# Optimization experiments

Hardware: AMD Instinct MI355X
Metric: run time of the kernel (lower is better)

## Reference

```python
import jax, jax.numpy as jnp
import numpy as np

NUM_HEADS = 8
NUM_LEVELS = 4
NUM_POINTS = 4
EMBED = 256
HEAD_DIM = EMBED // NUM_HEADS
SPATIAL = [(100, 100), (50, 50), (25, 25), (13, 13)]  # (H, W) per level


def _bilinear_sample(val, grid):
    """torch.nn.functional.grid_sample(mode='bilinear', padding_mode='zeros', align_corners=False).
    val: [B, H, W, C], grid: [B, N, 2] with (x, y) in [-1, 1]. Returns [B, N, C]."""
    B, H, W, C = val.shape
    x = (grid[..., 0] + 1.0) * (W * 0.5) - 0.5
    y = (grid[..., 1] + 1.0) * (H * 0.5) - 0.5
    x0 = jnp.floor(x)
    y0 = jnp.floor(y)
    wx1 = x - x0
    wy1 = y - y0
    wx0 = 1.0 - wx1
    wy0 = 1.0 - wy1
    x0i = x0.astype(jnp.int32)
    y0i = y0.astype(jnp.int32)
    valf = val.reshape(B, H * W, C)

    def corner(xi, yi, w):
        valid = (xi >= 0) & (xi < W) & (yi >= 0) & (yi < H)
        idx = jnp.clip(yi, 0, H - 1) * W + jnp.clip(xi, 0, W - 1)
        v = jnp.take_along_axis(valf, idx[..., None], axis=1)  # [B, N, C]
        return v * (w * valid)[..., None]

    return (corner(x0i, y0i, wx0 * wy0) + corner(x0i + 1, y0i, wx1 * wy0)
            + corner(x0i, y0i + 1, wx0 * wy1) + corner(x0i + 1, y0i + 1, wx1 * wy1))


def setup_inputs() -> dict:
    key = jax.random.key(0)
    ks = jax.random.split(key, 12)
    bs, nq = 4, 6000
    nv = sum(h * w for h, w in SPATIAL)
    s = 0.02
    return {
        "query": jax.random.normal(ks[0], (bs, nq, EMBED), jnp.float32),
        "value": jax.random.normal(ks[1], (bs, nv, EMBED), jnp.float32),
        "reference_points": jax.random.uniform(ks[2], (bs, nq, NUM_LEVELS, 2), jnp.float32),
        "W_off": jax.random.normal(ks[3], (EMBED, NUM_HEADS * NUM_LEVELS * NUM_POINTS * 2), jnp.float32) * s,
        "b_off": jax.random.normal(ks[4], (NUM_HEADS * NUM_LEVELS * NUM_POINTS * 2,), jnp.float32),
        "W_attn": jax.random.normal(ks[5], (EMBED, NUM_HEADS * NUM_LEVELS * NUM_POINTS), jnp.float32) * s,
        "b_attn": jnp.zeros((NUM_HEADS * NUM_LEVELS * NUM_POINTS,), jnp.float32),
        "W_val": jax.random.normal(ks[6], (EMBED, EMBED), jnp.float32) * s,
        "b_val": jnp.zeros((EMBED,), jnp.float32),
        "W_out": jax.random.normal(ks[7], (EMBED, EMBED), jnp.float32) * s,
        "b_out": jnp.zeros((EMBED,), jnp.float32),
        "spatial_shapes": jnp.asarray(np.array(SPATIAL, dtype=np.int32)),
    }


def reference(query, value, reference_points, W_off, b_off, W_attn, b_attn,
              W_val, b_val, W_out, b_out, spatial_shapes):
    shapes = [(int(h), int(w)) for h, w in np.asarray(spatial_shapes)]
    bs, nq, _ = query.shape
    nv = value.shape[1]

    v = (value @ W_val + b_val).reshape(bs, nv, NUM_HEADS, HEAD_DIM)
    offsets = (query @ W_off + b_off).reshape(bs, nq, NUM_HEADS, NUM_LEVELS, NUM_POINTS, 2)
    aw = (query @ W_attn + b_attn).reshape(bs, nq, NUM_HEADS, NUM_LEVELS * NUM_POINTS)
    aw = jax.nn.softmax(aw, axis=-1).reshape(bs, nq, NUM_HEADS, NUM_LEVELS, NUM_POINTS)

    # offset normalizer is [W, H] per level
    norm = jnp.asarray([[w, h] for h, w in shapes], dtype=query.dtype)  # [L, 2]
    loc = reference_points[:, :, None, :, None, :] + offsets / norm[None, None, None, :, None, :]
    grids = 2.0 * loc - 1.0  # [bs, nq, H, L, P, 2]
    # -> [bs*H, nq*P, 2] per level
    grids = jnp.transpose(grids, (0, 2, 1, 3, 4, 5)).reshape(bs * NUM_HEADS, nq, NUM_LEVELS, NUM_POINTS, 2)

    v_bh = jnp.transpose(v, (0, 2, 1, 3)).reshape(bs * NUM_HEADS, nv, HEAD_DIM)
    sampled = []
    start = 0
    for l, (H_, W_) in enumerate(shapes):
        val_l = v_bh[:, start:start + H_ * W_].reshape(bs * NUM_HEADS, H_, W_, HEAD_DIM)
        grid_l = grids[:, :, l].reshape(bs * NUM_HEADS, nq * NUM_POINTS, 2)
        s_l = _bilinear_sample(val_l, grid_l).reshape(bs * NUM_HEADS, nq, NUM_POINTS, HEAD_DIM)
        sampled.append(s_l)
        start += H_ * W_
    sampled = jnp.stack(sampled, axis=2)  # [bs*H, nq, L, P, c]

    aw_bh = jnp.transpose(aw, (0, 2, 1, 3, 4)).reshape(bs * NUM_HEADS, nq, NUM_LEVELS, NUM_POINTS)
    out = (sampled * aw_bh[..., None]).sum(axis=(2, 3))  # [bs*H, nq, c]
    out = out.reshape(bs, NUM_HEADS, nq, HEAD_DIM).transpose(0, 2, 1, 3).reshape(bs, nq, EMBED)
    out = out @ W_out + b_out
    return out + query
```

## Files before the change

kernel.cpp:

```cpp
#include <hip/hip_runtime.h>
#include <hip/hip_bf16.h>

#define BS 4
#define NQ 6000
#define NV 13294
#define NH 8
#define HD 32
#define EMB 256
#define MV (BS * NV)
#define MQ (BS * NQ)

typedef __attribute__((ext_vector_type(8))) short short8;
typedef __attribute__((ext_vector_type(4))) float floatx4;

__device__ __constant__ float LVL_DIM[4] = {100.f, 50.f, 25.f, 13.f};

__device__ inline unsigned short bf16bits(float f) {
  __hip_bfloat16 h = __float2bfloat16(f);
  return *reinterpret_cast<unsigned short*>(&h);
}
__device__ inline unsigned int pk2bf(float lo, float hi) {
  return (unsigned int)bf16bits(lo) | ((unsigned int)bf16bits(hi) << 16);
}
__device__ inline float bflo(unsigned int u) { return __uint_as_float(u << 16); }
__device__ inline float bfhi(unsigned int u) { return __uint_as_float(u & 0xffff0000u); }

#define LDSTR 40
#define TILEU (128 * LDSTR)

__global__ __launch_bounds__(256) void wtrans_kernel(
    const float* __restrict__ W_val, const float* __restrict__ W_off,
    const float* __restrict__ W_attn, const float* __restrict__ W_out,
    unsigned short* __restrict__ Wt_val, unsigned short* __restrict__ Wt_qcat,
    unsigned short* __restrict__ Wt_out) {
  __shared__ float tile[32][33];
  const int b = blockIdx.x;
  const int x = threadIdx.x & 31, ty = threadIdx.x >> 5;

  const float* src;
  unsigned short* dst;
  int k0, n0;
  if (b < 64) {
    src = W_val;
    dst = Wt_val;
    k0 = (b >> 3) * 32;
    n0 = (b & 7) * 32;
  } else if (b < 128) {
    const int bb = b - 64;
    src = W_off;
    dst = Wt_qcat;
    k0 = (bb >> 3) * 32;
    n0 = (bb & 7) * 32;
  } else if (b < 160) {
    const int bb = b - 128;
    src = W_attn;
    dst = Wt_qcat + 256 * EMB;
    k0 = (bb >> 2) * 32;
    n0 = (bb & 3) * 32;
#pragma unroll
    for (int i = 0; i < 4; ++i)
      tile[ty + 8 * i][x] = src[(size_t)(k0 + ty + 8 * i) * 128 + n0 + x];
    __syncthreads();
#pragma unroll
    for (int i = 0; i < 4; ++i)
      dst[(size_t)(n0 + ty + 8 * i) * EMB + k0 + x] =
          bf16bits(tile[x][ty + 8 * i]);
    return;
  } else {
    const int bb = b - 160;
    src = W_out;
    dst = Wt_out;
    k0 = (bb >> 3) * 32;
    n0 = (bb & 7) * 32;
  }
#pragma unroll
  for (int i = 0; i < 4; ++i)
    tile[ty + 8 * i][x] = src[(size_t)(k0 + ty + 8 * i) * 256 + n0 + x];
  __syncthreads();
#pragma unroll
  for (int i = 0; i < 4; ++i)
    dst[(size_t)(n0 + ty + 8 * i) * EMB + k0 + x] = bf16bits(tile[x][ty + 8 * i]);
}

__device__ inline void loadA32(const float* __restrict__ A, int M, int m0,
                               int k0, int tid, float4 ra[4]) {
  const int r = tid >> 1, kh = (tid & 1) * 16;
  const int row = m0 + r;
  if (row < M) {
    const float* src = A + (size_t)row * EMB + k0 + kh;
#pragma unroll
    for (int j = 0; j < 4; ++j) ra[j] = *(const float4*)(src + 4 * j);
  } else {
#pragma unroll
    for (int j = 0; j < 4; ++j) ra[j] = make_float4(0.f, 0.f, 0.f, 0.f);
  }
}
__device__ inline void storeA32(unsigned short* lds, int tid,
                                const float4 ra[4]) {
  const int r = tid >> 1, kh = (tid & 1) * 16;
  unsigned short* dst = lds + r * LDSTR + kh;
  uint4 u0, u1;
  u0.x = pk2bf(ra[0].x, ra[0].y);
  u0.y = pk2bf(ra[0].z, ra[0].w);
  u0.z = pk2bf(ra[1].x, ra[1].y);
  u0.w = pk2bf(ra[1].z, ra[1].w);
  u1.x = pk2bf(ra[2].x, ra[2].y);
  u1.y = pk2bf(ra[2].z, ra[2].w);
  u1.z = pk2bf(ra[3].x, ra[3].y);
  u1.w = pk2bf(ra[3].z, ra[3].w);
  *(uint4*)(dst) = u0;
  *(uint4*)(dst + 8) = u1;
}
__device__ inline void loadBb(const unsigned short* __restrict__ B, int NB,
                              int n0, int k0, int tid, uint4 rb[2]) {
  const int r = tid >> 1, kh = (tid & 1) * 16;
  const int row = n0 + r;
  if (row < NB) {
    const unsigned short* src = B + (size_t)row * EMB + k0 + kh;
    rb[0] = *(const uint4*)(src);
    rb[1] = *(const uint4*)(src + 8);
  } else {
    rb[0] = make_uint4(0, 0, 0, 0);
    rb[1] = make_uint4(0, 0, 0, 0);
  }
}
__device__ inline void storeBb(unsigned short* lds, int tid,
                               const uint4 rb[2]) {
  const int r = tid >> 1, kh = (tid & 1) * 16;
  unsigned short* dst = lds + r * LDSTR + kh;
  *(uint4*)(dst) = rb[0];
  *(uint4*)(dst + 8) = rb[1];
}

__device__ inline void mfma_step32(const unsigned short* ldsA,
                                   const unsigned short* ldsB, int wm, int wn,
                                   int lane, floatx4 acc[4][4]) {
  const unsigned short* ap =
      ldsA + (wm * 64 + (lane & 15)) * LDSTR + (lane >> 4) * 8;
  const unsigned short* bp =
      ldsB + (wn * 64 + (lane & 15)) * LDSTR + (lane >> 4) * 8;
  short8 af[4], bfr[4];
#pragma unroll
  for (int t = 0; t < 4; ++t) {
    af[t] = *(const short8*)(ap + t * 16 * LDSTR);
    bfr[t] = *(const short8*)(bp + t * 16 * LDSTR);
  }
#pragma unroll
  for (int mt = 0; mt < 4; ++mt)
#pragma unroll
    for (int nt = 0; nt < 4; ++nt)
      acc[mt][nt] = __builtin_amdgcn_mfma_f32_16x16x32_bf16(af[mt], bfr[nt],
                                                            acc[mt][nt], 0, 0, 0);
}

__device__ inline void gemm_loop32_f32A(const float* __restrict__ A, int M,
                                        int m0,
                                        const unsigned short* __restrict__ B,
                                        int NB, int n0, unsigned short* lds,
                                        int tid, int wm, int wn, int lane,
                                        floatx4 acc[4][4]) {
  unsigned short* bufA[2] = {lds, lds + 2 * TILEU};
  unsigned short* bufB[2] = {lds + TILEU, lds + 3 * TILEU};
  float4 sa[2][4];
  uint4 sb[2][2];
  loadA32(A, M, m0, 0, tid, sa[0]);
  loadBb(B, NB, n0, 0, tid, sb[0]);
  loadA32(A, M, m0, 32, tid, sa[1]);
  loadBb(B, NB, n0, 32, tid, sb[1]);
  storeA32(bufA[0], tid, sa[0]);
  storeBb(bufB[0], tid, sb[0]);
  __syncthreads();
#pragma unroll
  for (int k = 0; k < 8; ++k) {
    const int cur = k & 1, nxt = cur ^ 1;
    if (k + 2 < 8) {
      loadA32(A, M, m0, (k + 2) * 32, tid, sa[k & 1]);
      loadBb(B, NB, n0, (k + 2) * 32, tid, sb[k & 1]);
    }
    if (k + 1 < 8) {
      storeA32(bufA[nxt], tid, sa[(k + 1) & 1]);
      storeBb(bufB[nxt], tid, sb[(k + 1) & 1]);
    }
    mfma_step32(bufA[cur], bufB[cur], wm, wn, lane, acc);
    __syncthreads();
  }
}

__device__ inline void gemm_loop32_bf16A(const unsigned short* __restrict__ A,
                                         int M, int m0,
                                         const unsigned short* __restrict__ B,
                                         int NB, int n0, unsigned short* lds,
                                         int tid, int wm, int wn, int lane,
                                         floatx4 acc[4][4]) {
  unsigned short* bufA[2] = {lds, lds + 2 * TILEU};
  unsigned short* bufB[2] = {lds + TILEU, lds + 3 * TILEU};
  uint4 sa[2][2], sb[2][2];
  loadBb(A, M, m0, 0, tid, sa[0]);
  loadBb(B, NB, n0, 0, tid, sb[0]);
  loadBb(A, M, m0, 32, tid, sa[1]);
  loadBb(B, NB, n0, 32, tid, sb[1]);
  storeBb(bufA[0], tid, sa[0]);
  storeBb(bufB[0], tid, sb[0]);
  __syncthreads();
#pragma unroll
  for (int k = 0; k < 8; ++k) {
    const int cur = k & 1, nxt = cur ^ 1;
    if (k + 2 < 8) {
      loadBb(A, M, m0, (k + 2) * 32, tid, sa[k & 1]);
      loadBb(B, NB, n0, (k + 2) * 32, tid, sb[k & 1]);
    }
    if (k + 1 < 8) {
      storeBb(bufA[nxt], tid, sa[(k + 1) & 1]);
      storeBb(bufB[nxt], tid, sb[(k + 1) & 1]);
    }
    mfma_step32(bufA[cur], bufB[cur], wm, wn, lane, acc);
    __syncthreads();
  }
}

__global__ __launch_bounds__(256, 2) void vqproj_kernel(
    const float* __restrict__ value, const unsigned short* __restrict__ Wt_val,
    const float* __restrict__ b_val, unsigned short* __restrict__ vbh,
    const float* __restrict__ query, const unsigned short* __restrict__ Wt_qcat,
    const float* __restrict__ refpts, const float* __restrict__ b_off,
    const float* __restrict__ b_attn, float* __restrict__ locbuf,
    float* __restrict__ awbuf) {
  __shared__ unsigned short lds[4 * TILEU];
  const int tid = threadIdx.x, lane = tid & 63, w = tid >> 6;
  const int wm = w >> 1, wn = w & 1;
  floatx4 acc[4][4];
  const floatx4 zero = {0.f, 0.f, 0.f, 0.f};
#pragma unroll
  for (int i2 = 0; i2 < 4; i2++)
#pragma unroll
    for (int j = 0; j < 4; j++) acc[i2][j] = zero;
  const int quad = lane >> 4, cl = lane & 15;

  if (blockIdx.x < 832) {
    const int chunk = blockIdx.x >> 4, i = blockIdx.x & 15;
    const int m0 = (chunk * 8 + (i & 7)) * 128;
    const int n0 = (i >> 3) * 128;
    gemm_loop32_f32A(value, MV, m0, Wt_val, 256, n0, lds, tid, wm, wn, lane,
                     acc);
#pragma unroll
    for (int mt = 0; mt < 4; ++mt) {
#pragma unroll
      for (int r = 0; r < 4; ++r) {
        const int row = m0 + wm * 64 + mt * 16 + quad * 4 + r;
        if (row < MV) {
          const int b = row / NV, n = row - b * NV;
#pragma unroll
          for (int nt = 0; nt < 4; ++nt) {
            const int c = n0 + wn * 64 + nt * 16 + cl;
            const int h = c >> 5, d = c & 31;
            vbh[(((size_t)(b * NH + h)) * NV + n) * HD + d] =
                bf16bits(acc[mt][nt][r] + b_val[c]);
          }
        }
      }
    }
  } else {
    const int bid = blockIdx.x - 832;
    const int chunk = bid / 24, i = bid % 24;
    const int m_idx = chunk * 8 + (i & 7);
    if (m_idx >= 188) return;
    const int m0 = m_idx * 128;
    const int n0 = (i >> 3) * 128;
    gemm_loop32_f32A(query, MQ, m0, Wt_qcat, 384, n0, lds, tid, wm, wn, lane,
                     acc);
    if (n0 < 256) {
#pragma unroll
      for (int mt = 0; mt < 4; ++mt) {
#pragma unroll
        for (int r = 0; r < 4; ++r) {
          const int row = m0 + wm * 64 + mt * 16 + quad * 4 + r;
          if (row < MQ) {
#pragma unroll
            for (int nt = 0; nt < 4; ++nt) {
              const int c = n0 + wn * 64 + nt * 16 + cl;
              const int xy = c & 1, l = (c >> 3) & 3;
              const float dim = LVL_DIM[l];
              const float ref = refpts[(size_t)row * 8 + l * 2 + xy];
              locbuf[(size_t)row * 256 + c] =
                  ref * dim + acc[mt][nt][r] + b_off[c] - 0.5f;
            }
          }
        }
      }
    } else {
#pragma unroll
      for (int mt = 0; mt < 4; ++mt) {
#pragma unroll
        for (int r = 0; r < 4; ++r) {
          const int row = m0 + wm * 64 + mt * 16 + quad * 4 + r;
          if (row < MQ) {
#pragma unroll
            for (int nt = 0; nt < 4; ++nt) {
              const int ca = wn * 64 + nt * 16 + cl;
              awbuf[(size_t)row * 128 + ca] = acc[mt][nt][r] + b_attn[ca];
            }
          }
        }
      }
    }
  }
}

__global__ __launch_bounds__(256, 4) void sample_kernel(
    const unsigned short* __restrict__ vbh, const float* __restrict__ locbuf,
    const float* __restrict__ awbuf, unsigned short* __restrict__ sampledb) {
  const int blk = blockIdx.x;
  const int t = blk >> 3;
  const int quarter = t / 375;
  const int j = t - quarter * 375;
  const int slice = (blk & 7) * 4 + quarter;
  const int h = slice & 7;
  const int w = threadIdx.x >> 6;
  const int lane = threadIdx.x & 63;
  const int r0 = (slice >> 3) * NQ + j * 16 + w * 4;
  const int g = lane >> 2;
  const int d8 = lane & 3;
  const int l = g >> 2;

  const int W_ = (l < 2) ? ((l == 0) ? 100 : 50) : ((l == 2) ? 25 : 13);
  const int START = (l < 2) ? ((l == 0) ? 0 : 10000) : ((l == 2) ? 12500 : 13125);
  const unsigned int* base =
      (const unsigned int*)vbh + ((size_t)slice * NV + START) * 16 + d8 * 4;

  float acc[4][8];
#pragma unroll
  for (int rr = 0; rr < 4; ++rr) {
    const int row = r0 + rr;
    const float2 xy =
        *(const float2*)(locbuf + (size_t)row * 256 + h * 32 + g * 2);
    const float wl = awbuf[(size_t)row * 128 + h * 16 + g];
    float mx = wl;
    mx = fmaxf(mx, __shfl_xor(mx, 4));
    mx = fmaxf(mx, __shfl_xor(mx, 8));
    mx = fmaxf(mx, __shfl_xor(mx, 16));
    mx = fmaxf(mx, __shfl_xor(mx, 32));
    const float e = __expf(wl - mx);
    float ssum = e;
    ssum += __shfl_xor(ssum, 4);
    ssum += __shfl_xor(ssum, 8);
    ssum += __shfl_xor(ssum, 16);
    ssum += __shfl_xor(ssum, 32);
    const float wgt = e / ssum;

    const float fx = floorf(xy.x), fy = floorf(xy.y);
    const int x0 = (int)fx, y0 = (int)fy;
    const float wx1 = xy.x - fx, wy1 = xy.y - fy;
    const float wx0 = 1.f - wx1, wy0 = 1.f - wy1;
    const int x0c = min(max(x0, 0), W_ - 1), x1c = min(max(x0 + 1, 0), W_ - 1);
    const int y0c = min(max(y0, 0), W_ - 1), y1c = min(max(y0 + 1, 0), W_ - 1);
    const float mx0 = ((unsigned)x0 < (unsigned)W_) ? wx0 : 0.f;
    const float mx1 = ((unsigned)(x0 + 1) < (unsigned)W_) ? wx1 : 0.f;
    const float my0 = ((unsigned)y0 < (unsigned)W_) ? wy0 : 0.f;
    const float my1 = ((unsigned)(y0 + 1) < (unsigned)W_) ? wy1 : 0.f;
    const float wy0w = wgt * my0, wy1w = wgt * my1;
    const float w00 = wy0w * mx0, w01 = wy0w * mx1;
    const float w10 = wy1w * mx0, w11 = wy1w * mx1;

    const int rb0 = y0c * W_, rb1 = y1c * W_;
    const uint4 u00 = *(const uint4*)(base + (size_t)(rb0 + x0c) * 16);
    const uint4 u01 = *(const uint4*)(base + (size_t)(rb0 + x1c) * 16);
    const uint4 u10 = *(const uint4*)(base + (size_t)(rb1 + x0c) * 16);
    const uint4 u11 = *(const uint4*)(base + (size_t)(rb1 + x1c) * 16);
    const unsigned int* p00 = &u00.x;
    const unsigned int* p01 = &u01.x;
    const unsigned int* p10 = &u10.x;
    const unsigned int* p11 = &u11.x;
#pragma unroll
    for (int k = 0; k < 4; ++k) {
      acc[rr][2 * k] = w00 * bflo(p00[k]) + w01 * bflo(p01[k]) +
                       w10 * bflo(p10[k]) + w11 * bflo(p11[k]);
      acc[rr][2 * k + 1] = w00 * bfhi(p00[k]) + w01 * bfhi(p01[k]) +
                           w10 * bfhi(p10[k]) + w11 * bfhi(p11[k]);
    }
  }

  const bool b0 = (lane >> 2) & 1;
  const bool b1 = (lane >> 3) & 1;
  const bool b2 = (lane >> 4) & 1;
#pragma unroll
  for (int rr = 0; rr < 4; ++rr) {
    float* v = acc[rr];
#pragma unroll
    for (int jj = 0; jj < 4; ++jj) {
      float lo = v[jj], hi = v[jj + 4];
      float recv = __shfl_xor(b0 ? lo : hi, 4);
      v[jj] = (b0 ? hi : lo) + recv;
    }
#pragma unroll
    for (int jj = 0; jj < 2; ++jj) {
      float lo = v[jj], hi = v[jj + 2];
      float recv = __shfl_xor(b1 ? lo : hi, 8);
      v[jj] = (b1 ? hi : lo) + recv;
    }
    {
      float lo = v[0], hi = v[1];
      float recv = __shfl_xor(b2 ? lo : hi, 16);
      v[0] = (b2 ? hi : lo) + recv;
    }
    v[0] += __shfl_xor(v[0], 32);
  }

  const int dim = d8 * 8 + (b0 ? 4 : 0) + (b1 ? 2 : 0) + (b2 ? 1 : 0);
  const bool hi = (lane >= 32);
  const float v0 = hi ? acc[1][0] : acc[0][0];
  const float v1 = hi ? acc[3][0] : acc[2][0];
  const int row0 = r0 + (hi ? 1 : 0);
  const int row1 = r0 + 2 + (hi ? 1 : 0);
  sampledb[(size_t)row0 * EMB + h * 32 + dim] = bf16bits(v0);
  sampledb[(size_t)row1 * EMB + h * 32 + dim] = bf16bits(v1);
}

__global__ __launch_bounds__(256, 2) void oproj_kernel(
    const unsigned short* __restrict__ sampledb,
    const unsigned short* __restrict__ Wt, const float* __restrict__ b_out,
    const float* __restrict__ query, float* __restrict__ out) {
  __shared__ unsigned short lds[4 * TILEU];
  const int tid = threadIdx.x, lane = tid & 63, w = tid >> 6;
  const int wm = w >> 1, wn = w & 1;
  const int chunk = blockIdx.x >> 4, i = blockIdx.x & 15;
  const int m_idx = chunk * 8 + (i & 7);
  if (m_idx >= 188) return;
  const int m0 = m_idx * 128;
  const int n0 = (i >> 3) * 128;
  floatx4 acc[4][4];
  const floatx4 zero = {0.f, 0.f, 0.f, 0.f};
#pragma unroll
  for (int i2 = 0; i2 < 4; i2++)
#pragma unroll
    for (int j = 0; j < 4; j++) acc[i2][j] = zero;

  gemm_loop32_bf16A(sampledb, MQ, m0, Wt, 256, n0, lds, tid, wm, wn, lane,
                    acc);

  const int quad = lane >> 4, cl = lane & 15;
#pragma unroll
  for (int mt = 0; mt < 4; ++mt) {
#pragma unroll
    for (int r = 0; r < 4; ++r) {
      const int row = m0 + wm * 64 + mt * 16 + quad * 4 + r;
      if (row < MQ) {
#pragma unroll
        for (int nt = 0; nt < 4; ++nt) {
          const int c = n0 + wn * 64 + nt * 16 + cl;
          out[(size_t)row * EMB + c] =
              acc[mt][nt][r] + b_out[c] + query[(size_t)row * EMB + c];
        }
      }
    }
  }
}

extern "C" void kernel_launch(void* const* d_in, const int* in_sizes, int n_in,
                              void* d_out, int out_size, void* d_ws,
                              size_t ws_size, hipStream_t stream) {
  const float* query  = (const float*)d_in[0];
  const float* value  = (const float*)d_in[1];
  const float* refpts = (const float*)d_in[2];
  const float* W_off  = (const float*)d_in[3];
  const float* b_off  = (const float*)d_in[4];
  const float* W_attn = (const float*)d_in[5];
  const float* b_attn = (const float*)d_in[6];
  const float* W_val  = (const float*)d_in[7];
  const float* b_val  = (const float*)d_in[8];
  const float* W_out  = (const float*)d_in[9];
  const float* b_out  = (const float*)d_in[10];
  float* out = (float*)d_out;

  char* ws = (char*)d_ws;
  unsigned short* vbh = (unsigned short*)ws;
  float* locbuf = (float*)(ws + 27226112);
  float* awbuf = (float*)(ws + 51802112);
  unsigned short* sampledb = (unsigned short*)(ws + 64090112);
  unsigned short* Wt_val = (unsigned short*)(ws + 76378112);
  unsigned short* Wt_qcat = (unsigned short*)(ws + 76509184);
  unsigned short* Wt_out = (unsigned short*)(ws + 76705792);

  wtrans_kernel<<<224, 256, 0, stream>>>(W_val, W_off, W_attn, W_out, Wt_val,
                                         Wt_qcat, Wt_out);
  vqproj_kernel<<<1408, 256, 0, stream>>>(value, Wt_val, b_val, vbh, query,
                                          Wt_qcat, refpts, b_off, b_attn,
                                          locbuf, awbuf);
  sample_kernel<<<12000, 256, 0, stream>>>(vbh, locbuf, awbuf, sampledb);
  oproj_kernel<<<384, 256, 0, stream>>>(sampledb, Wt_out, b_out, query, out);
}
```

Baseline: 236.7 us.

## Stage value-projection epilogue through LDS and retile output projection to 64-row blocks

The value projection epilogue now writes the bf16 results into shared memory first, then issues 16-byte coalesced stores into the per-head vbh layout instead of scattered 2-byte stores. The output projection kernel is retiled to 64x128 blocks of 128 threads (750 blocks instead of 384 with idle tail blocks), with a custom double-buffered load path. This gives more blocks for load balance across CUs at the cost of less B-tile reuse per block and an extra LDS round trip plus barrier in the vqproj epilogue.

```diff
diff --git a/kernel.cpp b/kernel.cpp
--- a/kernel.cpp
+++ b/kernel.cpp
@@ -27,6 +27,7 @@
 
 #define LDSTR 40
 #define TILEU (128 * LDSTR)
+#define OSTR 136
 
 __global__ __launch_bounds__(256) void wtrans_kernel(
     const float* __restrict__ W_val, const float* __restrict__ W_off,
@@ -186,38 +187,6 @@
   }
 }
 
-__device__ inline void gemm_loop32_bf16A(const unsigned short* __restrict__ A,
-                                         int M, int m0,
-                                         const unsigned short* __restrict__ B,
-                                         int NB, int n0, unsigned short* lds,
-                                         int tid, int wm, int wn, int lane,
-                                         floatx4 acc[4][4]) {
-  unsigned short* bufA[2] = {lds, lds + 2 * TILEU};
-  unsigned short* bufB[2] = {lds + TILEU, lds + 3 * TILEU};
-  uint4 sa[2][2], sb[2][2];
-  loadBb(A, M, m0, 0, tid, sa[0]);
-  loadBb(B, NB, n0, 0, tid, sb[0]);
-  loadBb(A, M, m0, 32, tid, sa[1]);
-  loadBb(B, NB, n0, 32, tid, sb[1]);
-  storeBb(bufA[0], tid, sa[0]);
-  storeBb(bufB[0], tid, sb[0]);
-  __syncthreads();
-#pragma unroll
-  for (int k = 0; k < 8; ++k) {
-    const int cur = k & 1, nxt = cur ^ 1;
-    if (k + 2 < 8) {
-      loadBb(A, M, m0, (k + 2) * 32, tid, sa[k & 1]);
-      loadBb(B, NB, n0, (k + 2) * 32, tid, sb[k & 1]);
-    }
-    if (k + 1 < 8) {
-      storeBb(bufA[nxt], tid, sa[(k + 1) & 1]);
-      storeBb(bufB[nxt], tid, sb[(k + 1) & 1]);
-    }
-    mfma_step32(bufA[cur], bufB[cur], wm, wn, lane, acc);
-    __syncthreads();
-  }
-}
-
 __global__ __launch_bounds__(256, 2) void vqproj_kernel(
     const float* __restrict__ value, const unsigned short* __restrict__ Wt_val,
     const float* __restrict__ b_val, unsigned short* __restrict__ vbh,
@@ -242,21 +211,32 @@
     const int n0 = (i >> 3) * 128;
     gemm_loop32_f32A(value, MV, m0, Wt_val, 256, n0, lds, tid, wm, wn, lane,
                      acc);
+    unsigned short* slds = lds;
 #pragma unroll
     for (int mt = 0; mt < 4; ++mt) {
 #pragma unroll
       for (int r = 0; r < 4; ++r) {
-        const int row = m0 + wm * 64 + mt * 16 + quad * 4 + r;
-        if (row < MV) {
-          const int b = row / NV, n = row - b * NV;
-#pragma unroll
-          for (int nt = 0; nt < 4; ++nt) {
-            const int c = n0 + wn * 64 + nt * 16 + cl;
-            const int h = c >> 5, d = c & 31;
-            vbh[(((size_t)(b * NH + h)) * NV + n) * HD + d] =
-                bf16bits(acc[mt][nt][r] + b_val[c]);
-          }
+        const int rl = wm * 64 + mt * 16 + quad * 4 + r;
+#pragma unroll
+        for (int nt = 0; nt < 4; ++nt) {
+          const int col = wn * 64 + nt * 16 + cl;
+          slds[rl * OSTR + col] = bf16bits(acc[mt][nt][r] + b_val[n0 + col]);
         }
+      }
+    }
+    __syncthreads();
+    const int piece = tid & 3;
+#pragma unroll
+    for (int p = 0; p < 8; ++p) {
+      const int cid = p * 64 + (tid >> 2);
+      const int rl = cid >> 2, hh = cid & 3;
+      const int row = m0 + rl;
+      if (row < MV) {
+        const int b = row / NV, n = row - b * NV;
+        const int h = (n0 >> 5) + hh;
+        const uint4 v =
+            *(const uint4*)(slds + rl * OSTR + hh * 32 + piece * 8);
+        *(uint4*)(vbh + (((size_t)(b * NH + h)) * NV + n) * HD + piece * 8) = v;
       }
     }
   } else {
@@ -415,18 +395,18 @@
   sampledb[(size_t)row1 * EMB + h * 32 + dim] = bf16bits(v1);
 }
 
-__global__ __launch_bounds__(256, 2) void oproj_kernel(
+#define OA 0
+#define OB (64 * LDSTR)
+#define OA1 (192 * LDSTR)
+#define OB1 (256 * LDSTR)
+__global__ __launch_bounds__(128, 2) void oproj_kernel(
     const unsigned short* __restrict__ sampledb,
     const unsigned short* __restrict__ Wt, const float* __restrict__ b_out,
     const float* __restrict__ query, float* __restrict__ out) {
-  __shared__ unsigned short lds[4 * TILEU];
-  const int tid = threadIdx.x, lane = tid & 63, w = tid >> 6;
-  const int wm = w >> 1, wn = w & 1;
-  const int chunk = blockIdx.x >> 4, i = blockIdx.x & 15;
-  const int m_idx = chunk * 8 + (i & 7);
-  if (m_idx >= 188) return;
-  const int m0 = m_idx * 128;
-  const int n0 = (i >> 3) * 128;
+  __shared__ unsigned short lds[384 * LDSTR];
+  const int tid = threadIdx.x, lane = tid & 63, wn = tid >> 6;
+  const int m0 = (blockIdx.x >> 1) * 64;
+  const int n0 = (blockIdx.x & 1) * 128;
   floatx4 acc[4][4];
   const floatx4 zero = {0.f, 0.f, 0.f, 0.f};
 #pragma unroll
@@ -434,22 +414,65 @@
 #pragma unroll
     for (int j = 0; j < 4; j++) acc[i2][j] = zero;
 
-  gemm_loop32_bf16A(sampledb, MQ, m0, Wt, 256, n0, lds, tid, wm, wn, lane,
-                    acc);
+  unsigned short* bufA[2] = {lds + OA, lds + OA1};
+  unsigned short* bufB[2] = {lds + OB, lds + OB1};
+  uint4 sa[2][2], sb[2][4];
+#pragma unroll
+  for (int s = 0; s < 2; ++s) {
+    const int r = tid >> 1, kh = (tid & 1) * 16;
+    const unsigned short* asrc =
+        sampledb + (size_t)(m0 + r) * EMB + s * 32 + kh;
+    sa[s][0] = *(const uint4*)(asrc);
+    sa[s][1] = *(const uint4*)(asrc + 8);
+    const unsigned short* bsrc = Wt + (size_t)(n0 + tid) * EMB + s * 32;
+#pragma unroll
+    for (int j = 0; j < 4; ++j) sb[s][j] = *(const uint4*)(bsrc + 8 * j);
+  }
+  {
+    const int r = tid >> 1, kh = (tid & 1) * 16;
+    *(uint4*)(bufA[0] + r * LDSTR + kh) = sa[0][0];
+    *(uint4*)(bufA[0] + r * LDSTR + kh + 8) = sa[0][1];
+#pragma unroll
+    for (int j = 0; j < 4; ++j)
+      *(uint4*)(bufB[0] + tid * LDSTR + 8 * j) = sb[0][j];
+  }
+  __syncthreads();
+#pragma unroll
+  for (int k = 0; k < 8; ++k) {
+    const int cur = k & 1, nxt = cur ^ 1;
+    if (k + 2 < 8) {
+      const int r = tid >> 1, kh = (tid & 1) * 16;
+      const unsigned short* asrc =
+          sampledb + (size_t)(m0 + r) * EMB + (k + 2) * 32 + kh;
+      sa[k & 1][0] = *(const uint4*)(asrc);
+      sa[k & 1][1] = *(const uint4*)(asrc + 8);
+      const unsigned short* bsrc = Wt + (size_t)(n0 + tid) * EMB + (k + 2) * 32;
+#pragma unroll
+      for (int j = 0; j < 4; ++j) sb[k & 1][j] = *(const uint4*)(bsrc + 8 * j);
+    }
+    if (k + 1 < 8) {
+      const int r = tid >> 1, kh = (tid & 1) * 16;
+      *(uint4*)(bufA[nxt] + r * LDSTR + kh) = sa[(k + 1) & 1][0];
+      *(uint4*)(bufA[nxt] + r * LDSTR + kh + 8) = sa[(k + 1) & 1][1];
+#pragma unroll
+      for (int j = 0; j < 4; ++j)
+        *(uint4*)(bufB[nxt] + tid * LDSTR + 8 * j) = sb[(k + 1) & 1][j];
+    }
+    mfma_step32(bufA[cur], bufB[cur], 0, wn, lane, acc);
+    __syncthreads();
+  }
 
   const int quad = lane >> 4, cl = lane & 15;
 #pragma unroll
   for (int mt = 0; mt < 4; ++mt) {
 #pragma unroll
     for (int r = 0; r < 4; ++r) {
-      const int row = m0 + wm * 64 + mt * 16 + quad * 4 + r;
-      if (row < MQ) {
-#pragma unroll
-        for (int nt = 0; nt < 4; ++nt) {
-          const int c = n0 + wn * 64 + nt * 16 + cl;
-          out[(size_t)row * EMB + c] =
-              acc[mt][nt][r] + b_out[c] + query[(size_t)row * EMB + c];
-        }
+      const int row = m0 + mt * 16 + quad * 4 + r;
+#pragma unroll
+      for (int nt = 0; nt < 4; ++nt) {
+        const int c = n0 + wn * 64 + nt * 16 + cl;
+        out[(size_t)row * EMB + c] =
+            acc[mt][nt][r] + b_out[c] + query[(size_t)row * EMB + c];
       }
     }
   }
@@ -486,5 +509,5 @@
                                           Wt_qcat, refpts, b_off, b_attn,
                                           locbuf, awbuf);
   sample_kernel<<<12000, 256, 0, stream>>>(vbh, locbuf, awbuf, sampledb);
-  oproj_kernel<<<384, 256, 0, stream>>>(sampledb, Wt_out, b_out, query, out);
-}
+  oproj_kernel<<<750, 128, 0, stream>>>(sampledb, Wt_out, b_out, query, out);
+}
```

New measurement: 257.1 us. 8.6% more time.
